# Performance work log

Hardware: AMD Instinct MI355X
Metric: run time of the kernel (lower is better)

## Reference

```python
import jax, jax.numpy as jnp
import numpy as np

N_NODES = 100000
N_EDGES = 1600000
D_IN = 32
D_OUT = 64


def setup_inputs() -> dict:
    key = jax.random.key(0)
    ks = jax.random.split(key, 6)
    x = jax.random.normal(ks[0], (N_NODES, D_IN), dtype=jnp.float32)
    edge_row = jax.random.randint(ks[1], (N_EDGES,), 0, N_NODES, dtype=jnp.int32)
    edge_col = jax.random.randint(ks[2], (N_EDGES,), 0, N_NODES, dtype=jnp.int32)
    edge_val = jax.random.uniform(ks[3], (N_EDGES,), dtype=jnp.float32)
    W = jax.random.normal(ks[4], (D_IN, D_OUT), dtype=jnp.float32) * (1.0 / np.sqrt(D_IN))
    b = jax.random.normal(ks[5], (D_OUT,), dtype=jnp.float32) * 0.01
    return {"x": x, "edge_row": edge_row, "edge_col": edge_col,
            "edge_val": edge_val, "W": W, "b": b, "k": 4}


def _spmm(edge_row, edge_col, edge_val, x, n_nodes):
    # out[i] = sum_{e: row[e]==i} val[e] * x[col[e]]  (sparse adj @ x)
    gathered = edge_val[:, None] * x[edge_col]  # [E, D]
    return jax.ops.segment_sum(gathered, edge_row, num_segments=n_nodes)


def reference(x, edge_row, edge_col, edge_val, W, b, k):
    # k-hop propagation: x <- A @ x, repeated k times (k is a static Python int)
    for _ in range(k):
        x = _spmm(edge_row, edge_col, edge_val, x, N_NODES)
    # final dense linear: x @ W + b
    return x @ W + b
```

## Files before the change

kernel.cpp:

```cpp
#include <hip/hip_runtime.h>
#include <hip/hip_fp16.h>

#define N_NODES 100000
#define N_EDGES 1600000
#define D_IN 32
#define D_OUT 64

#define RPB 200
#define NBKT 500
#define CAP 4096
#define EPT 16
#define SCT 256
#define EPB (EPT * SCT)
#define SBLOCKS ((N_EDGES + EPB - 1) / EPB)

#define COL_BITS 17
#define COL_MASK ((1u << COL_BITS) - 1u)
#define VAL_SCALE 32767.0f
#define VAL_INV (1.0f / 32767.0f)

typedef unsigned int uv2 __attribute__((ext_vector_type(2)));

__global__ void init_bcur(int* __restrict__ bcur) {
    int i = threadIdx.x;
    if (i < NBKT) bcur[i] = i * CAP;
}

__global__ void scatter_chunks(const int* __restrict__ erow,
                               const int* __restrict__ ecol,
                               const float* __restrict__ eval_,
                               int* __restrict__ bcur,
                               int2* __restrict__ staged) {
    __shared__ int h[NBKT];
    __shared__ int cb[NBKT];
    for (int i = threadIdx.x; i < NBKT; i += blockDim.x) h[i] = 0;
    __syncthreads();
    int base = blockIdx.x * EPB;
    unsigned pk[EPT]; float val[EPT]; int brk[EPT];
#pragma unroll
    for (int k = 0; k < EPT; ++k) {
        int e = base + k * SCT + threadIdx.x;
        if (e < N_EDGES) {
            int r = __builtin_nontemporal_load(&erow[e]);
            int c = __builtin_nontemporal_load(&ecol[e]);
            float v = __builtin_nontemporal_load(&eval_[e]);
            int b = r / RPB;
            int rl = r - b * RPB;
            int rank = atomicAdd(&h[b], 1);
            pk[k] = ((unsigned)rl << COL_BITS) | (unsigned)c;
            val[k] = v;
            brk[k] = b | (rank << 9);
        } else brk[k] = -1;
    }
    __syncthreads();
    for (int i = threadIdx.x; i < NBKT; i += blockDim.x) {
        int c = h[i];
        if (c) cb[i] = atomicAdd(&bcur[i], c);
    }
    __syncthreads();
#pragma unroll
    for (int k = 0; k < EPT; ++k) {
        if (brk[k] >= 0) {
            int b = brk[k] & 511;
            int rank = brk[k] >> 9;
            int2 p; p.x = (int)pk[k]; p.y = __float_as_int(val[k]);
            staged[cb[b] + rank] = p;
        }
    }
}

__global__ void sort_bucket(const int* __restrict__ bcur,
                            const int2* __restrict__ staged,
                            unsigned int* __restrict__ epack,
                            int2* __restrict__ row_rng) {
    __shared__ int hist[RPB];
    __shared__ int offs[RPB];
    __shared__ int cur[RPB];
    int b = blockIdx.x;
    int s0 = b * CAP, s1 = bcur[b];
    for (int i = threadIdx.x; i < RPB; i += blockDim.x) hist[i] = 0;
    __syncthreads();
    for (int e = s0 + threadIdx.x; e < s1; e += blockDim.x) {
        unsigned w = (unsigned)staged[e].x;
        atomicAdd(&hist[w >> COL_BITS], 1);
    }
    __syncthreads();
    if (threadIdx.x == 0) {
        int run = 0;
        for (int i = 0; i < RPB; ++i) { offs[i] = run; run += hist[i]; }
    }
    __syncthreads();
    int r0 = b * RPB;
    for (int i = threadIdx.x; i < RPB; i += blockDim.x) {
        int st = s0 + offs[i];
        int2 rr; rr.x = st; rr.y = st + hist[i];
        row_rng[r0 + i] = rr;
        cur[i] = offs[i];
    }
    __syncthreads();
    for (int e = s0 + threadIdx.x; e < s1; e += blockDim.x) {
        int2 p = staged[e];
        unsigned w = (unsigned)p.x;
        int rl = (int)(w >> COL_BITS);
        int pos = atomicAdd(&cur[rl], 1);
        float v = __int_as_float(p.y);
        unsigned q = (unsigned)(int)(v * VAL_SCALE + 0.5f);
        epack[s0 + pos] = (q << COL_BITS) | (w & COL_MASK);
    }
}

__global__ void f32_to_f16(const float2* __restrict__ in, unsigned int* __restrict__ out) {
    int i = blockIdx.x * blockDim.x + threadIdx.x;
    const int n2 = N_NODES * D_IN / 2;
    if (i < n2) {
        float2 f = in[i];
        __half2 h = __floats2half2_rn(f.x, f.y);
        out[i] = *(unsigned int*)&h;
    }
}

__global__ void spmm_csr(const int2* __restrict__ row_rng,
                         const unsigned int* __restrict__ epack,
                         const uv2* __restrict__ xin,
                         uv2* __restrict__ xout) {
    int lane = threadIdx.x & 63;
    int wave = threadIdx.x >> 6;
    int qt = lane >> 4;
    int g  = (lane >> 3) & 1;
    int j  = lane & 7;
    int r = (blockIdx.x * (blockDim.x >> 6) + wave) * 4 + qt;
    if (r >= N_NODES) return;
    int2 pe = row_rng[r];
    int p0 = pe.x, p1 = pe.y;
    float4 a0 = {0.f,0.f,0.f,0.f}, a1 = {0.f,0.f,0.f,0.f};
    float4 a2 = {0.f,0.f,0.f,0.f}, a3 = {0.f,0.f,0.f,0.f};
    for (int eb = p0; eb < p1; eb += 8) {
        int i0 = eb + g, i1 = eb + 2 + g, i2 = eb + 4 + g, i3 = eb + 6 + g;
        unsigned q0 = (i0 < p1) ? epack[i0] : 0u;
        unsigned q1 = (i1 < p1) ? epack[i1] : 0u;
        unsigned q2 = (i2 < p1) ? epack[i2] : 0u;
        unsigned q3 = (i3 < p1) ? epack[i3] : 0u;
        uv2 w0 = xin[(q0 & COL_MASK) * 8 + j];
        uv2 w1 = xin[(q1 & COL_MASK) * 8 + j];
        uv2 w2 = xin[(q2 & COL_MASK) * 8 + j];
        uv2 w3 = xin[(q3 & COL_MASK) * 8 + j];
        float v0 = (float)(q0 >> COL_BITS) * VAL_INV;
        float v1 = (float)(q1 >> COL_BITS) * VAL_INV;
        float v2 = (float)(q2 >> COL_BITS) * VAL_INV;
        float v3 = (float)(q3 >> COL_BITS) * VAL_INV;
        unsigned w0x = w0.x, w0y = w0.y, w1x = w1.x, w1y = w1.y;
        unsigned w2x = w2.x, w2y = w2.y, w3x = w3.x, w3y = w3.y;
        float2 f0a = __half22float2(*(__half2*)&w0x), f0b = __half22float2(*(__half2*)&w0y);
        float2 f1a = __half22float2(*(__half2*)&w1x), f1b = __half22float2(*(__half2*)&w1y);
        float2 f2a = __half22float2(*(__half2*)&w2x), f2b = __half22float2(*(__half2*)&w2y);
        float2 f3a = __half22float2(*(__half2*)&w3x), f3b = __half22float2(*(__half2*)&w3y);
        a0.x += v0 * f0a.x; a0.y += v0 * f0a.y; a0.z += v0 * f0b.x; a0.w += v0 * f0b.y;
        a1.x += v1 * f1a.x; a1.y += v1 * f1a.y; a1.z += v1 * f1b.x; a1.w += v1 * f1b.y;
        a2.x += v2 * f2a.x; a2.y += v2 * f2a.y; a2.z += v2 * f2b.x; a2.w += v2 * f2b.y;
        a3.x += v3 * f3a.x; a3.y += v3 * f3a.y; a3.z += v3 * f3b.x; a3.w += v3 * f3b.y;
    }
    float4 acc;
    acc.x = (a0.x + a1.x) + (a2.x + a3.x);
    acc.y = (a0.y + a1.y) + (a2.y + a3.y);
    acc.z = (a0.z + a1.z) + (a2.z + a3.z);
    acc.w = (a0.w + a1.w) + (a2.w + a3.w);
    acc.x += __shfl_xor(acc.x, 8, 64);
    acc.y += __shfl_xor(acc.y, 8, 64);
    acc.z += __shfl_xor(acc.z, 8, 64);
    acc.w += __shfl_xor(acc.w, 8, 64);
    if (g == 0) {
        __half2 o0 = __floats2half2_rn(acc.x, acc.y);
        __half2 o1 = __floats2half2_rn(acc.z, acc.w);
        uv2 w;
        w.x = *(unsigned int*)&o0;
        w.y = *(unsigned int*)&o1;
        xout[r * 8 + j] = w;
    }
}

__global__ void linear_bias(const __half2* __restrict__ xin,
                            const float* __restrict__ W,
                            const float* __restrict__ b,
                            float* __restrict__ out) {
    __shared__ float sW[D_IN * D_OUT];
    __shared__ float sb[D_OUT];
    for (int i = threadIdx.x; i < D_IN * D_OUT; i += blockDim.x) sW[i] = W[i];
    if (threadIdx.x < D_OUT) sb[threadIdx.x] = b[threadIdx.x];
    __syncthreads();

    int r = blockIdx.x * 4 + (threadIdx.x >> 6);
    int j = threadIdx.x & 63;
    if (r >= N_NODES) return;

    const __half2* xr = xin + r * (D_IN / 2);
    float acc = sb[j];
#pragma unroll
    for (int d = 0; d < D_IN / 2; ++d) {
        float2 f = __half22float2(xr[d]);
        acc += f.x * sW[(2 * d) * D_OUT + j] + f.y * sW[(2 * d + 1) * D_OUT + j];
    }
    out[r * D_OUT + j] = acc;
}

extern "C" void kernel_launch(void* const* d_in, const int* in_sizes, int n_in,
                              void* d_out, int out_size, void* d_ws, size_t ws_size,
                              hipStream_t stream) {
    const float* x     = (const float*)d_in[0];
    const int*   erow  = (const int*)d_in[1];
    const int*   ecol  = (const int*)d_in[2];
    const float* eval_ = (const float*)d_in[3];
    const float* W     = (const float*)d_in[4];
    const float* b     = (const float*)d_in[5];
    float* out = (float*)d_out;

    unsigned int* xh0 = (unsigned int*)d_ws;
    unsigned int* xh1 = xh0 + (size_t)N_NODES * D_IN / 2;
    int* bcur = (int*)(xh1 + (size_t)N_NODES * D_IN / 2);
    int2* row_rng = (int2*)(bcur + 512);
    int2* staged = row_rng + N_NODES;
    unsigned int* epack = (unsigned int*)(staged + (size_t)NBKT * CAP);

    const int threads = 256;

    init_bcur<<<1, 512, 0, stream>>>(bcur);
    scatter_chunks<<<SBLOCKS, SCT, 0, stream>>>(erow, ecol, eval_, bcur, staged);
    sort_bucket<<<NBKT, threads, 0, stream>>>(bcur, staged, epack, row_rng);

    const int n2e = N_NODES * D_IN / 2;
    f32_to_f16<<<(n2e + threads - 1) / threads, threads, 0, stream>>>((const float2*)x, xh0);

    const int rows_per_block = (threads / 64) * 4;
    const int sblocks = (N_NODES + rows_per_block - 1) / rows_per_block;
    const unsigned int* cur = xh0;
    for (int hop = 0; hop < 4; ++hop) {
        unsigned int* dst = (hop & 1) ? xh0 : xh1;
        spmm_csr<<<sblocks, threads, 0, stream>>>((const int2*)row_rng, epack,
                                                  (const uv2*)cur, (uv2*)dst);
        cur = dst;
    }

    const int lin_blocks = (N_NODES + 3) / 4;
    linear_bias<<<lin_blocks, 256, 0, stream>>>((const __half2*)cur, W, b, out);
}
```

Before: 251.4 us.

## Pad CSR rows to multiples of eight and fuse fp16 conversion into scatter

Each row's edge range is padded to a multiple of eight with zeroed entries. The SpMM inner loop can then fetch four packed edges with one 16-byte vector load and no per-edge bounds checks. The separate fp32-to-fp16 conversion kernel is folded into extra blocks of the scatter kernel, which removes one launch. Padding adds zero-weight gathers of node 0 and stretches each bucket's footprint, which relies on the padded bucket still fitting within CAP.

```diff
diff --git a/kernel.cpp b/kernel.cpp
--- a/kernel.cpp
+++ b/kernel.cpp
@@ -13,6 +13,8 @@
 #define SCT 256
 #define EPB (EPT * SCT)
 #define SBLOCKS ((N_EDGES + EPB - 1) / EPB)
+#define N2 (N_NODES * D_IN / 2)
+#define CVT_BLOCKS ((N2 + 255) / 256)
 
 #define COL_BITS 17
 #define COL_MASK ((1u << COL_BITS) - 1u)
@@ -20,6 +22,7 @@
 #define VAL_INV (1.0f / 32767.0f)
 
 typedef unsigned int uv2 __attribute__((ext_vector_type(2)));
+typedef unsigned int uv4 __attribute__((ext_vector_type(4)));
 
 __global__ void init_bcur(int* __restrict__ bcur) {
     int i = threadIdx.x;
@@ -30,7 +33,18 @@
                                const int* __restrict__ ecol,
                                const float* __restrict__ eval_,
                                int* __restrict__ bcur,
-                               int2* __restrict__ staged) {
+                               int2* __restrict__ staged,
+                               const float2* __restrict__ xf,
+                               unsigned int* __restrict__ xh) {
+    if (blockIdx.x >= SBLOCKS) {
+        int i = (blockIdx.x - SBLOCKS) * blockDim.x + threadIdx.x;
+        if (i < N2) {
+            float2 f = xf[i];
+            __half2 h = __floats2half2_rn(f.x, f.y);
+            xh[i] = *(unsigned int*)&h;
+        }
+        return;
+    }
     __shared__ int h[NBKT];
     __shared__ int cb[NBKT];
     for (int i = threadIdx.x; i < NBKT; i += blockDim.x) h[i] = 0;
@@ -76,6 +90,7 @@
     __shared__ int hist[RPB];
     __shared__ int offs[RPB];
     __shared__ int cur[RPB];
+    __shared__ int ptot;
     int b = blockIdx.x;
     int s0 = b * CAP, s1 = bcur[b];
     for (int i = threadIdx.x; i < RPB; i += blockDim.x) hist[i] = 0;
@@ -87,13 +102,19 @@
     __syncthreads();
     if (threadIdx.x == 0) {
         int run = 0;
-        for (int i = 0; i < RPB; ++i) { offs[i] = run; run += hist[i]; }
+        for (int i = 0; i < RPB; ++i) {
+            offs[i] = run;
+            run += (hist[i] + 7) & ~7;
+        }
+        ptot = run;
     }
     __syncthreads();
     int r0 = b * RPB;
+    int pt = ptot;
+    for (int i = threadIdx.x; i < pt; i += blockDim.x) epack[s0 + i] = 0u;
     for (int i = threadIdx.x; i < RPB; i += blockDim.x) {
         int st = s0 + offs[i];
-        int2 rr; rr.x = st; rr.y = st + hist[i];
+        int2 rr; rr.x = st; rr.y = st + ((hist[i] + 7) & ~7);
         row_rng[r0 + i] = rr;
         cur[i] = offs[i];
     }
@@ -109,18 +130,8 @@
     }
 }
 
-__global__ void f32_to_f16(const float2* __restrict__ in, unsigned int* __restrict__ out) {
-    int i = blockIdx.x * blockDim.x + threadIdx.x;
-    const int n2 = N_NODES * D_IN / 2;
-    if (i < n2) {
-        float2 f = in[i];
-        __half2 h = __floats2half2_rn(f.x, f.y);
-        out[i] = *(unsigned int*)&h;
-    }
-}
-
 __global__ void spmm_csr(const int2* __restrict__ row_rng,
-                         const unsigned int* __restrict__ epack,
+                         const uv4* __restrict__ epack4,
                          const uv2* __restrict__ xin,
                          uv2* __restrict__ xout) {
     int lane = threadIdx.x & 63;
@@ -135,11 +146,8 @@
     float4 a0 = {0.f,0.f,0.f,0.f}, a1 = {0.f,0.f,0.f,0.f};
     float4 a2 = {0.f,0.f,0.f,0.f}, a3 = {0.f,0.f,0.f,0.f};
     for (int eb = p0; eb < p1; eb += 8) {
-        int i0 = eb + g, i1 = eb + 2 + g, i2 = eb + 4 + g, i3 = eb + 6 + g;
-        unsigned q0 = (i0 < p1) ? epack[i0] : 0u;
-        unsigned q1 = (i1 < p1) ? epack[i1] : 0u;
-        unsigned q2 = (i2 < p1) ? epack[i2] : 0u;
-        unsigned q3 = (i3 < p1) ? epack[i3] : 0u;
+        uv4 q = epack4[(eb >> 2) + g];
+        unsigned q0 = q.x, q1 = q.y, q2 = q.z, q3 = q.w;
         uv2 w0 = xin[(q0 & COL_MASK) * 8 + j];
         uv2 w1 = xin[(q1 & COL_MASK) * 8 + j];
         uv2 w2 = xin[(q2 & COL_MASK) * 8 + j];
@@ -214,8 +222,8 @@
     float* out = (float*)d_out;
 
     unsigned int* xh0 = (unsigned int*)d_ws;
-    unsigned int* xh1 = xh0 + (size_t)N_NODES * D_IN / 2;
-    int* bcur = (int*)(xh1 + (size_t)N_NODES * D_IN / 2);
+    unsigned int* xh1 = xh0 + (size_t)N2;
+    int* bcur = (int*)(xh1 + (size_t)N2);
     int2* row_rng = (int2*)(bcur + 512);
     int2* staged = row_rng + N_NODES;
     unsigned int* epack = (unsigned int*)(staged + (size_t)NBKT * CAP);
@@ -223,18 +231,17 @@
     const int threads = 256;
 
     init_bcur<<<1, 512, 0, stream>>>(bcur);
-    scatter_chunks<<<SBLOCKS, SCT, 0, stream>>>(erow, ecol, eval_, bcur, staged);
+    scatter_chunks<<<SBLOCKS + CVT_BLOCKS, SCT, 0, stream>>>(
+        erow, ecol, eval_, bcur, staged, (const float2*)x, xh0);
     sort_bucket<<<NBKT, threads, 0, stream>>>(bcur, staged, epack, row_rng);
-
-    const int n2e = N_NODES * D_IN / 2;
-    f32_to_f16<<<(n2e + threads - 1) / threads, threads, 0, stream>>>((const float2*)x, xh0);
 
     const int rows_per_block = (threads / 64) * 4;
     const int sblocks = (N_NODES + rows_per_block - 1) / rows_per_block;
     const unsigned int* cur = xh0;
     for (int hop = 0; hop < 4; ++hop) {
         unsigned int* dst = (hop & 1) ? xh0 : xh1;
-        spmm_csr<<<sblocks, threads, 0, stream>>>((const int2*)row_rng, epack,
+        spmm_csr<<<sblocks, threads, 0, stream>>>((const int2*)row_rng,
+                                                  (const uv4*)epack,
                                                   (const uv2*)cur, (uv2*)dst);
         cur = dst;
     }
```

Result: faster. 243.4 us (-3.2%).
